# Kernel tuning notes

Hardware: AMD Instinct MI355X
Metric: run time of the kernel (lower is better)

The kernel has to match this reference:

```python
import jax, jax.numpy as jnp
import numpy as np

NUM_CHANNELS = 256
NUM_HEADS = 8
HEAD_DIM = NUM_CHANNELS // NUM_HEADS


def setup_inputs() -> dict:
    key = jax.random.key(0)
    k1, k2, k3, k4, k5 = jax.random.split(key, 5)
    C = NUM_CHANNELS
    s = 1.0 / np.sqrt(C)
    image = jax.random.normal(k1, (8, C, 32, 32), dtype=jnp.float32)
    # kqv_projection: Linear(C, 3C); mix_heads: Linear(C, C). Stored as [in, out].
    w_kqv = jax.random.uniform(k2, (C, 3 * C), minval=-s, maxval=s, dtype=jnp.float32)
    b_kqv = jax.random.uniform(k3, (3 * C,), minval=-s, maxval=s, dtype=jnp.float32)
    w_mix = jax.random.uniform(k4, (C, C), minval=-s, maxval=s, dtype=jnp.float32)
    b_mix = jax.random.uniform(k5, (C,), minval=-s, maxval=s, dtype=jnp.float32)
    return {"image": image, "w_kqv": w_kqv, "b_kqv": b_kqv, "w_mix": w_mix, "b_mix": b_mix}


def _masked_attention(seq, w_kqv, b_kqv, w_mix, b_mix):
    # seq: [N, T, C]
    N, T, C = seq.shape
    H, D = NUM_HEADS, HEAD_DIM
    projected = seq @ w_kqv + b_kqv            # [N, T, 3C]
    k, q, v = jnp.split(projected, 3, axis=-1)  # order: keys, queries, values
    # split heads -> [N, H, T, D]
    k = k.reshape(N, T, H, D).transpose(0, 2, 1, 3)
    q = q.reshape(N, T, H, D).transpose(0, 2, 1, 3)
    v = v.reshape(N, T, H, D).transpose(0, 2, 1, 3)
    logits = jnp.einsum('nhtd,nhsd->nhts', q, k) / jnp.sqrt(jnp.float32(D))
    causal = jnp.tril(jnp.ones((T, T), dtype=bool))
    logits = jnp.where(causal, logits, -jnp.inf)
    weights = jax.nn.softmax(logits, axis=-1)
    out = jnp.einsum('nhts,nhsd->nhtd', weights, v)  # [N, H, T, D]
    out = out.transpose(0, 2, 1, 3).reshape(N, T, C)  # combine heads
    return out @ w_mix + b_mix


def reference(image, w_kqv, b_kqv, w_mix, b_mix):
    N, C, Hh, Ww = image.shape
    seq = image.transpose(0, 2, 3, 1).reshape(N, Hh * Ww, C)
    attn = _masked_attention(seq, w_kqv, b_kqv, w_mix, b_mix)
    attn = attn.reshape(N, Hh, Ww, C).transpose(0, 3, 1, 2)
    return attn + image
```

## Files before the change

### kernel.cpp

```cpp
#include <hip/hip_runtime.h>
#include <math.h>

constexpr int NB  = 8;
constexpr int C   = 256;
constexpr int T   = 1024;
constexpr int NH  = 8;
constexpr int HD  = 32;
constexpr int C3  = 768;

constexpr float QSCALE = 0.25503489422229562f;

typedef __attribute__((ext_vector_type(8))) short bf16x8;
typedef __attribute__((ext_vector_type(4))) short bf16x4;
typedef __attribute__((ext_vector_type(4))) float f32x4;

__device__ inline short f2bf(float f) {
    unsigned u = __float_as_uint(f);
    u += 0x7FFF + ((u >> 16) & 1);
    return (short)(u >> 16);
}
__device__ inline short f2bf_trunc(float f) {
    return (short)(__float_as_uint(f) >> 16);
}

__device__ __forceinline__ f32x4 mfma16(bf16x4 a, bf16x4 b, f32x4 c) {
    return __builtin_amdgcn_mfma_f32_16x16x16bf16_1k(a, b, c, 0, 0, 0);
}

__device__ __forceinline__ void gl16(const void* g, void* l) {
    __builtin_amdgcn_global_load_lds(
        (const __attribute__((address_space(1))) unsigned int*)g,
        (__attribute__((address_space(3))) unsigned int*)l, 16, 0, 0);
}

__global__ __launch_bounds__(256) void prep_tc(const float* __restrict__ image,
                                               const float* __restrict__ wkqv,
                                               const float* __restrict__ wmix,
                                               short* __restrict__ Xb,
                                               short* __restrict__ Wkb,
                                               short* __restrict__ Wmb) {
    __shared__ float tile[64][65];
    const int bid = blockIdx.x;
    const int tid = threadIdx.x;
    const float* src; short* dst;
    int Cc, r0, c0;
    if (bid < 512) {
        const int nb = bid >> 6, t = bid & 63;
        src = image + (size_t)nb * C * T;
        dst = Xb + (size_t)nb * T * C;
        Cc = T; r0 = (t & 3) * 64; c0 = (t >> 2) * 64;
    } else if (bid < 560) {
        const int t = bid - 512;
        src = wkqv; dst = Wkb;
        Cc = C3; r0 = (t & 3) * 64; c0 = (t >> 2) * 64;
    } else {
        const int t = bid - 560;
        src = wmix; dst = Wmb;
        Cc = C; r0 = (t & 3) * 64; c0 = (t >> 2) * 64;
    }
    const int lr = tid >> 4, lc = (tid & 15) * 4;
    #pragma unroll
    for (int p = 0; p < 4; ++p) {
        float4 v = *(const float4*)&src[(size_t)(r0 + 16 * p + lr) * Cc + c0 + lc];
        tile[16 * p + lr][lc + 0] = v.x;
        tile[16 * p + lr][lc + 1] = v.y;
        tile[16 * p + lr][lc + 2] = v.z;
        tile[16 * p + lr][lc + 3] = v.w;
    }
    __syncthreads();
    const int wc = tid >> 2, wr = (tid & 3) * 16;
    bf16x8 v0, v1;
    #pragma unroll
    for (int e = 0; e < 8; ++e) v0[e] = f2bf(tile[wr + e][wc]);
    #pragma unroll
    for (int e = 0; e < 8; ++e) v1[e] = f2bf(tile[wr + 8 + e][wc]);
    short* o = dst + (size_t)(c0 + wc) * C + r0 + wr;
    *(bf16x8*)&o[0] = v0;
    *(bf16x8*)&o[8] = v1;
}

__global__ __launch_bounds__(256) void kqv_mfma(const short* __restrict__ Xb,
                                                const short* __restrict__ Wkb,
                                                const float* __restrict__ bkqv,
                                                short* __restrict__ Kb,
                                                short* __restrict__ Qb,
                                                short* __restrict__ Vtb) {
    __shared__ __align__(16) short As[2][128 * 64];
    __shared__ __align__(16) short Bs[2][64 * 64];
    const int tid = threadIdx.x;
    const int n0 = blockIdx.x * 64;
    const int m0 = blockIdx.y * 128;
    const int nb = m0 >> 10, t0 = m0 & 1023;
    const int wv = tid >> 6, lane = tid & 63;
    const int m = lane & 15, quad = lane >> 4;

    const short* Xn = Xb + (size_t)nb * T * C + (size_t)t0 * C;
    const short* Wn = Wkb + (size_t)n0 * C;

    f32x4 acc[2][4];
    const f32x4 z = {0.f, 0.f, 0.f, 0.f};
    #pragma unroll
    for (int i = 0; i < 2; ++i)
        #pragma unroll
        for (int j = 0; j < 4; ++j) acc[i][j] = z;

    const int sx = (m & 7) << 4;

    auto stage = [&](int buf, int k0) {
        #pragma unroll
        for (int p = 0; p < 4; ++p) {
            const int o = p * 4096 + tid * 16;
            const int row = o >> 7;
            const int cb = (o & 127) ^ ((row & 7) << 4);
            gl16(Xn + (size_t)row * C + k0 + (cb >> 1), (char*)As[buf] + o);
        }
        #pragma unroll
        for (int p = 0; p < 2; ++p) {
            const int o = p * 4096 + tid * 16;
            const int row = o >> 7;
            const int cb = (o & 127) ^ ((row & 7) << 4);
            gl16(Wn + (size_t)row * C + k0 + (cb >> 1), (char*)Bs[buf] + o);
        }
    };

    stage(0, 0);
    __syncthreads();
    int cur = 0;
    for (int t = 0; t < 4; ++t) {
        if (t < 3) stage(cur ^ 1, 64 * (t + 1));

        bf16x8 a[2][2], b[2][4];
        #pragma unroll
        for (int kk = 0; kk < 2; ++kk) {
            #pragma unroll
            for (int i = 0; i < 2; ++i)
                a[kk][i] = *(const bf16x8*)((const char*)As[cur] +
                            (32 * wv + 16 * i + m) * 128 + ((kk * 64 + quad * 16) ^ sx));
            #pragma unroll
            for (int j = 0; j < 4; ++j)
                b[kk][j] = *(const bf16x8*)((const char*)Bs[cur] +
                            (16 * j + m) * 128 + ((kk * 64 + quad * 16) ^ sx));
        }
        #pragma unroll
        for (int kk = 0; kk < 2; ++kk)
            #pragma unroll
            for (int i = 0; i < 2; ++i)
                #pragma unroll
                for (int j = 0; j < 4; ++j)
                    acc[i][j] = __builtin_amdgcn_mfma_f32_16x16x32_bf16(a[kk][i], b[kk][j], acc[i][j], 0, 0, 0);

        if (t < 3) __syncthreads();
        cur ^= 1;
    }

    #pragma unroll
    for (int j = 0; j < 4; ++j) {
        int jj = n0 + 16 * j + m;
        int chunk = jj >> 8, hh = (jj >> 5) & 7, d = jj & 31;
        float bias = bkqv[jj];
        if (chunk < 2) {
            short* dst = (chunk == 0) ? Kb : Qb;
            float mul = (chunk == 1) ? QSCALE : 1.0f;
            size_t base = (size_t)(nb * NH + hh) * T * HD + d;
            #pragma unroll
            for (int i = 0; i < 2; ++i) {
                int t = t0 + 32 * wv + 16 * i + 4 * quad;
                #pragma unroll
                for (int r = 0; r < 4; ++r)
                    dst[base + (size_t)(t + r) * HD] = f2bf((acc[i][j][r] + bias) * mul);
            }
        } else {
            size_t base = (size_t)(nb * NH + hh) * (16 * 2048) + (size_t)d * 64;
            #pragma unroll
            for (int i = 0; i < 2; ++i) {
                #pragma unroll
                for (int r = 0; r < 4; ++r) {
                    int t = t0 + 32 * wv + 16 * i + 4 * quad + r;
                    Vtb[base + (size_t)(t >> 6) * 2048 + (t & 63)] = f2bf(acc[i][j][r] + bias);
                }
            }
        }
    }
}

__global__ __launch_bounds__(256) void attn_mfma(const short* __restrict__ Kb,
                                                 const short* __restrict__ Qb,
                                                 const short* __restrict__ Vtb,
                                                 short* __restrict__ attnb) {
    const int qb = (blockIdx.z & 4) ? 7 - blockIdx.x : blockIdx.x;
    const int h  = blockIdx.y;
    const int nb = blockIdx.z;
    const int tid  = threadIdx.x;
    const int wv   = tid >> 6;
    const int lane = tid & 63;
    const int m    = lane & 15;
    const int quad = lane >> 4;

    const int q0  = qb * 128;
    const int nst = 2 * qb + 2;
    const size_t hb = (size_t)(nb * NH + h) * T * HD;
    const short* Kp = Kb + hb;
    const short* Qp = Qb + hb;
    const short* Vp = Vtb + (size_t)(nb * NH + h) * (16 * 2048);
    const f32x4 z = {0.f, 0.f, 0.f, 0.f};

    bf16x8 aq[2];
    #pragma unroll
    for (int i = 0; i < 2; ++i)
        aq[i] = *(const bf16x8*)&Qp[(size_t)(q0 + 32 * wv + 16 * i + m) * HD + 8 * quad];

    bf16x8 bk[4];
    bf16x4 vb[4][2];
    #pragma unroll
    for (int j = 0; j < 4; ++j)
        bk[j] = *(const bf16x8*)&Kp[(size_t)(16 * j + m) * HD + 8 * quad];
    #pragma unroll
    for (int j = 0; j < 4; ++j)
        #pragma unroll
        for (int hf = 0; hf < 2; ++hf)
            vb[j][hf] = *(const bf16x4*)&Vp[(size_t)(16 * hf + m) * 64 + 16 * j + 4 * quad];

    f32x4 O[2][2] = {{z, z}, {z, z}};
    float lp[2] = {0.f, 0.f};

    auto step = [&](const int st, const bool msk) {
        f32x4 S[2][4];
        #pragma unroll
        for (int i = 0; i < 2; ++i)
            #pragma unroll
            for (int j = 0; j < 4; ++j)
                S[i][j] = __builtin_amdgcn_mfma_f32_16x16x32_bf16(bk[j], aq[i], z, 0, 0, 0);

        if (st + 1 < nst) {
            #pragma unroll
            for (int j = 0; j < 4; ++j)
                bk[j] = *(const bf16x8*)&Kp[(size_t)((st + 1) * 64 + 16 * j + m) * HD + 8 * quad];
        }

        const int s0 = st * 64;
        bf16x4 pa[2][4];
        #pragma unroll
        for (int i = 0; i < 2; ++i) {
            const int qr = q0 + 32 * wv + 16 * i + m;
            #pragma unroll
            for (int j = 0; j < 4; ++j) {
                const int kb = s0 + 16 * j + 4 * quad;
                #pragma unroll
                for (int r = 0; r < 4; ++r) {
                    float e = __builtin_amdgcn_exp2f(S[i][j][r]);
                    if (msk && kb + r > qr) e = 0.f;
                    lp[i] += e;
                    pa[i][j][r] = f2bf_trunc(e);
                }
            }
        }

        #pragma unroll
        for (int j = 0; j < 4; ++j)
            #pragma unroll
            for (int i = 0; i < 2; ++i) {
                O[i][0] = mfma16(pa[i][j], vb[j][0], O[i][0]);
                O[i][1] = mfma16(pa[i][j], vb[j][1], O[i][1]);
            }

        if (st + 1 < nst) {
            const short* Vn = Vp + (size_t)(st + 1) * 2048;
            #pragma unroll
            for (int j = 0; j < 4; ++j)
                #pragma unroll
                for (int hf = 0; hf < 2; ++hf)
                    vb[j][hf] = *(const bf16x4*)&Vn[(size_t)(16 * hf + m) * 64 + 16 * j + 4 * quad];
        }
    };

    const int mq = 2 * qb;
    for (int st = 0; st < mq; ++st) step(st, false);
    step(mq, true);
    step(mq + 1, true);

    #pragma unroll
    for (int i = 0; i < 2; ++i) {
        float l = lp[i];
        l += __shfl_xor(l, 16);
        l += __shfl_xor(l, 32);
        #pragma unroll
        for (int r = 0; r < 4; ++r) {
            float lr = __shfl(l, 4 * quad + r);
            float inv = 1.f / lr;
            int row = q0 + 32 * wv + 16 * i + 4 * quad + r;
            short* op = attnb + ((size_t)(nb * T + row)) * C + h * HD;
            op[m]      = f2bf(O[i][0][r] * inv);
            op[16 + m] = f2bf(O[i][1][r] * inv);
        }
    }
}

__global__ __launch_bounds__(256) void mix_mfma(const short* __restrict__ attnb,
                                                const short* __restrict__ Wmb,
                                                const float* __restrict__ bmix,
                                                const float* __restrict__ image,
                                                float* __restrict__ out) {
    __shared__ __align__(16) short Bs[64][264];
    const int tid = threadIdx.x;
    const int n0 = blockIdx.x * 64;
    const int m0 = blockIdx.y * 64;
    const int nb = m0 >> 10, t0 = m0 & 1023;
    const int wv = tid >> 6, lane = tid & 63;
    const int m = lane & 15, quad = lane >> 4;

    {
        const short* wrow = Wmb + (size_t)(n0 + (tid >> 2)) * C + (tid & 3) * 64;
        short* brow = &Bs[tid >> 2][(tid & 3) * 64];
        #pragma unroll
        for (int g = 0; g < 8; ++g)
            *(bf16x8*)&brow[8 * g] = *(const bf16x8*)&wrow[8 * g];
    }
    __syncthreads();

    f32x4 acc[4];
    const f32x4 z = {0.f, 0.f, 0.f, 0.f};
    #pragma unroll
    for (int j = 0; j < 4; ++j) acc[j] = z;

    #pragma unroll
    for (int k0 = 0; k0 < C; k0 += 32) {
        bf16x8 a = *(const bf16x8*)&attnb[(size_t)(m0 + 16 * wv + m) * C + k0 + 8 * quad];
        bf16x8 b[4];
        #pragma unroll
        for (int j = 0; j < 4; ++j) b[j] = *(const bf16x8*)&Bs[16 * j + m][k0 + 8 * quad];
        #pragma unroll
        for (int j = 0; j < 4; ++j)
            acc[j] = __builtin_amdgcn_mfma_f32_16x16x32_bf16(a, b[j], acc[j], 0, 0, 0);
    }

    const int tb = t0 + 16 * wv + 4 * quad;
    #pragma unroll
    for (int j = 0; j < 4; ++j) {
        int c = n0 + 16 * j + m;
        float bias = bmix[c];
        size_t o = (size_t)(nb * C + c) * T + tb;
        float4 img = *(const float4*)&image[o];
        float4 res = { acc[j][0] + bias + img.x,
                       acc[j][1] + bias + img.y,
                       acc[j][2] + bias + img.z,
                       acc[j][3] + bias + img.w };
        *(float4*)&out[o] = res;
    }
}

extern "C" void kernel_launch(void* const* d_in, const int* in_sizes, int n_in,
                              void* d_out, int out_size, void* d_ws, size_t ws_size,
                              hipStream_t stream) {
    const float* image = (const float*)d_in[0];
    const float* w_kqv = (const float*)d_in[1];
    const float* b_kqv = (const float*)d_in[2];
    const float* w_mix = (const float*)d_in[3];
    const float* b_mix = (const float*)d_in[4];
    float* out = (float*)d_out;

    short* Xb    = (short*)d_ws;
    short* Wkb   = Xb  + (size_t)NB * T * C;
    short* Wmb   = Wkb + (size_t)C3 * C;
    short* Kb    = Wmb + (size_t)C * C;
    short* Qb    = Kb  + (size_t)NB * NH * T * HD;
    short* Vtb   = Qb  + (size_t)NB * NH * T * HD;
    short* attnb = Vtb + (size_t)NB * NH * T * HD;

    prep_tc<<<576, 256, 0, stream>>>(image, w_kqv, w_mix, Xb, Wkb, Wmb);
    kqv_mfma<<<dim3(C3 / 64, NB * T / 128), 256, 0, stream>>>(Xb, Wkb, b_kqv, Kb, Qb, Vtb);
    attn_mfma<<<dim3(8, NH, NB), 256, 0, stream>>>(Kb, Qb, Vtb, attnb);
    mix_mfma<<<dim3(C / 64, NB * T / 64), 256, 0, stream>>>(attnb, Wmb, b_mix, image, out);
}
```

Measured before the change: 111.2 us.

## Single-buffer the KQV GEMM staging and split softmax row-sum accumulators

The KQV projection kernel drops double-buffered LDS staging and instead loads each K-slice into one buffer, synchronizes, computes, and synchronizes again. This halves its shared memory footprint, which may allow more resident blocks, but loads no longer overlap compute. In the attention kernel, the per-element serial row-sum accumulation is replaced with a pairwise tree sum into two partial accumulators per row. This shortens the dependency chain of the adds and slightly changes floating-point summation order.

```diff
diff --git a/kernel.cpp b/kernel.cpp
--- a/kernel.cpp
+++ b/kernel.cpp
@@ -85,8 +85,8 @@
                                                 short* __restrict__ Kb,
                                                 short* __restrict__ Qb,
                                                 short* __restrict__ Vtb) {
-    __shared__ __align__(16) short As[2][128 * 64];
-    __shared__ __align__(16) short Bs[2][64 * 64];
+    __shared__ __align__(16) short As[128 * 64];
+    __shared__ __align__(16) short Bs[64 * 64];
     const int tid = threadIdx.x;
     const int n0 = blockIdx.x * 64;
     const int m0 = blockIdx.y * 128;
@@ -106,39 +106,33 @@
 
     const int sx = (m & 7) << 4;
 
-    auto stage = [&](int buf, int k0) {
+    for (int k0 = 0; k0 < C; k0 += 64) {
         #pragma unroll
         for (int p = 0; p < 4; ++p) {
             const int o = p * 4096 + tid * 16;
             const int row = o >> 7;
             const int cb = (o & 127) ^ ((row & 7) << 4);
-            gl16(Xn + (size_t)row * C + k0 + (cb >> 1), (char*)As[buf] + o);
+            gl16(Xn + (size_t)row * C + k0 + (cb >> 1), (char*)As + o);
         }
         #pragma unroll
         for (int p = 0; p < 2; ++p) {
             const int o = p * 4096 + tid * 16;
             const int row = o >> 7;
             const int cb = (o & 127) ^ ((row & 7) << 4);
-            gl16(Wn + (size_t)row * C + k0 + (cb >> 1), (char*)Bs[buf] + o);
-        }
-    };
-
-    stage(0, 0);
-    __syncthreads();
-    int cur = 0;
-    for (int t = 0; t < 4; ++t) {
-        if (t < 3) stage(cur ^ 1, 64 * (t + 1));
+            gl16(Wn + (size_t)row * C + k0 + (cb >> 1), (char*)Bs + o);
+        }
+        __syncthreads();
 
         bf16x8 a[2][2], b[2][4];
         #pragma unroll
         for (int kk = 0; kk < 2; ++kk) {
             #pragma unroll
             for (int i = 0; i < 2; ++i)
-                a[kk][i] = *(const bf16x8*)((const char*)As[cur] +
+                a[kk][i] = *(const bf16x8*)((const char*)As +
                             (32 * wv + 16 * i + m) * 128 + ((kk * 64 + quad * 16) ^ sx));
             #pragma unroll
             for (int j = 0; j < 4; ++j)
-                b[kk][j] = *(const bf16x8*)((const char*)Bs[cur] +
+                b[kk][j] = *(const bf16x8*)((const char*)Bs +
                             (16 * j + m) * 128 + ((kk * 64 + quad * 16) ^ sx));
         }
         #pragma unroll
@@ -148,9 +142,7 @@
                 #pragma unroll
                 for (int j = 0; j < 4; ++j)
                     acc[i][j] = __builtin_amdgcn_mfma_f32_16x16x32_bf16(a[kk][i], b[kk][j], acc[i][j], 0, 0, 0);
-
-        if (t < 3) __syncthreads();
-        cur ^= 1;
+        __syncthreads();
     }
 
     #pragma unroll
@@ -221,7 +213,7 @@
             vb[j][hf] = *(const bf16x4*)&Vp[(size_t)(16 * hf + m) * 64 + 16 * j + 4 * quad];
 
     f32x4 O[2][2] = {{z, z}, {z, z}};
-    float lp[2] = {0.f, 0.f};
+    float lp[2][2] = {{0.f, 0.f}, {0.f, 0.f}};
 
     auto step = [&](const int st, const bool msk) {
         f32x4 S[2][4];
@@ -245,13 +237,21 @@
             #pragma unroll
             for (int j = 0; j < 4; ++j) {
                 const int kb = s0 + 16 * j + 4 * quad;
-                #pragma unroll
-                for (int r = 0; r < 4; ++r) {
-                    float e = __builtin_amdgcn_exp2f(S[i][j][r]);
-                    if (msk && kb + r > qr) e = 0.f;
-                    lp[i] += e;
-                    pa[i][j][r] = f2bf_trunc(e);
+                float e0 = __builtin_amdgcn_exp2f(S[i][j][0]);
+                float e1 = __builtin_amdgcn_exp2f(S[i][j][1]);
+                float e2 = __builtin_amdgcn_exp2f(S[i][j][2]);
+                float e3 = __builtin_amdgcn_exp2f(S[i][j][3]);
+                if (msk) {
+                    if (kb + 0 > qr) e0 = 0.f;
+                    if (kb + 1 > qr) e1 = 0.f;
+                    if (kb + 2 > qr) e2 = 0.f;
+                    if (kb + 3 > qr) e3 = 0.f;
                 }
+                pa[i][j][0] = f2bf_trunc(e0);
+                pa[i][j][1] = f2bf_trunc(e1);
+                pa[i][j][2] = f2bf_trunc(e2);
+                pa[i][j][3] = f2bf_trunc(e3);
+                lp[i][j & 1] += (e0 + e1) + (e2 + e3);
             }
         }
 
@@ -280,7 +280,7 @@
 
     #pragma unroll
     for (int i = 0; i < 2; ++i) {
-        float l = lp[i];
+        float l = lp[i][0] + lp[i][1];
         l += __shfl_xor(l, 16);
         l += __shfl_xor(l, 32);
         #pragma unroll
```

New measurement: 110.9 us. Within noise of the previous version (-0.3%).
